# Optimization experiments

Measured on AMD Instinct MI355X. Metric: run time of the kernel, lower is better.

## Reference

```python
import jax, jax.numpy as jnp
import numpy as np

N = 50000
E = 800000
F_IN = 128
F_OUT = 128


def setup_inputs() -> dict:
    key = jax.random.key(0)
    ks = jax.random.split(key, 7)
    feature = jax.random.normal(ks[0], (N, F_IN), dtype=jnp.float32)
    self_weight = jax.random.uniform(ks[1], (N, 1), dtype=jnp.float32)
    weight = jax.random.uniform(ks[2], (E,), dtype=jnp.float32)
    src = jax.random.randint(ks[3], (E,), 0, N, dtype=jnp.int32)
    dst = jax.random.randint(ks[4], (E,), 0, N, dtype=jnp.int32)
    W = jax.random.normal(ks[5], (F_OUT, F_IN), dtype=jnp.float32) / np.sqrt(F_IN)
    b = jax.random.normal(ks[6], (F_OUT,), dtype=jnp.float32) * 0.01
    return {"feature": feature, "self_weight": self_weight, "weight": weight,
            "src": src, "dst": dst, "W": W, "b": b}


def reference(feature, self_weight, weight, src, dst, W, b):
    # messages: (w + 1) * h_src  -> [E, F_IN]
    msgs = (weight + 1.0)[:, None] * feature[src]
    # segment-sum into destination nodes -> [N, F_IN]
    agg = jax.ops.segment_sum(msgs, dst, num_segments=N)
    # self-loop affine: h * (self_weight + 1) + aggregated messages
    h = feature * (self_weight + 1.0) + agg
    # final linear: h @ W^T + b
    return h @ W.T + b
```

## Files before the change

### kernel.cpp

```cpp
#include <hip/hip_runtime.h>


#define F 128
#define NPB 32
#define CAPB 1024
#define CHUNK 4096
#define MAXNB 1600

typedef __attribute__((ext_vector_type(8))) short short8;
typedef __attribute__((ext_vector_type(4))) float f32x4;

__device__ inline unsigned short f2b(float f) {
    union { float f; unsigned u; } v; v.f = f;
    unsigned r = (v.u + 0x7fffu + ((v.u >> 16) & 1u)) >> 16;
    return (unsigned short)r;
}
__device__ inline float blo(unsigned u) { union { unsigned u; float f; } x; x.u = u << 16; return x.f; }
__device__ inline float bhi(unsigned u) { union { unsigned u; float f; } x; x.u = u & 0xffff0000u; return x.f; }

struct __align__(8) Edge { unsigned pk; float w; };

__global__ __launch_bounds__(256) void init_kernel(
    const float* __restrict__ W, unsigned short* __restrict__ wbf,
    int* __restrict__ gcur, int nb)
{
    int i = blockIdx.x * 256 + threadIdx.x;
    if (i < 4096) {
        float4 v = ((const float4*)W)[i];
        ushort4 h; h.x = f2b(v.x); h.y = f2b(v.y); h.z = f2b(v.z); h.w = f2b(v.w);
        ((ushort4*)wbf)[i] = h;
    } else if (i - 4096 < nb) {
        gcur[i - 4096] = 0;
    }
}

__global__ __launch_bounds__(256) void gemm_scatter(
    const float* __restrict__ feat, const unsigned short* __restrict__ wbf,
    const int* __restrict__ dst, const int* __restrict__ src,
    const float* __restrict__ weight,
    unsigned short* __restrict__ g, int* __restrict__ gcur,
    Edge* __restrict__ sorted, int M, int E, int SB, int NB)
{
    __shared__ __align__(16) char smem[128 * 136 * 2];
    const int tid = threadIdx.x;

    if ((int)blockIdx.x >= SB) {
        unsigned short* Wl = (unsigned short*)smem;
        const int row0 = ((int)blockIdx.x - SB) * 64;

        const int lane = tid & 63, wid = tid >> 6;
        const int m = lane & 15, quad = lane >> 4;
        const int rbase = wid * 16;
        int rr = row0 + rbase + m; if (rr >= M) rr = M - 1;
        const float* frow = feat + (size_t)rr * F;

        float4 a32[4][2];
#pragma unroll
        for (int kk = 0; kk < 4; ++kk) {
            a32[kk][0] = *(const float4*)&frow[kk * 32 + quad * 8];
            a32[kk][1] = *(const float4*)&frow[kk * 32 + quad * 8 + 4];
        }

        for (int i = tid; i < 2048; i += 256) {
            int r = i >> 4, c8 = i & 15;
            *(uint4*)&Wl[r * 136 + c8 * 8] = *(const uint4*)&wbf[r * 128 + c8 * 8];
        }

        short8 afrag[4];
#pragma unroll
        for (int kk = 0; kk < 4; ++kk) {
            afrag[kk][0] = (short)f2b(a32[kk][0].x);
            afrag[kk][1] = (short)f2b(a32[kk][0].y);
            afrag[kk][2] = (short)f2b(a32[kk][0].z);
            afrag[kk][3] = (short)f2b(a32[kk][0].w);
            afrag[kk][4] = (short)f2b(a32[kk][1].x);
            afrag[kk][5] = (short)f2b(a32[kk][1].y);
            afrag[kk][6] = (short)f2b(a32[kk][1].z);
            afrag[kk][7] = (short)f2b(a32[kk][1].w);
        }
        __syncthreads();

        f32x4 acc[8];
#pragma unroll
        for (int t = 0; t < 8; ++t) acc[t] = (f32x4){0.f, 0.f, 0.f, 0.f};

#pragma unroll
        for (int kk = 0; kk < 4; ++kk) {
            const int k0 = kk * 32 + quad * 8;
#pragma unroll
            for (int t = 0; t < 8; ++t) {
                short8 bfrag = *(const short8*)&Wl[(t * 16 + m) * 136 + k0];
                acc[t] = __builtin_amdgcn_mfma_f32_16x16x32_bf16(afrag[kk], bfrag, acc[t], 0, 0, 0);
            }
        }

#pragma unroll
        for (int reg = 0; reg < 4; ++reg) {
            int r = row0 + rbase + quad * 4 + reg;
            if (r < M) {
#pragma unroll
                for (int t = 0; t < 8; ++t)
                    g[(size_t)r * F + t * 16 + m] = f2b(acc[t][reg]);
            }
        }
    } else {
        int* hist  = (int*)smem;
        int* lbase = hist + MAXNB;
        const int e0 = (int)blockIdx.x * CHUNK;

        int dvals[CHUNK / 256];
        for (int i = tid; i < NB; i += 256) hist[i] = 0;
        __syncthreads();
#pragma unroll
        for (int j = 0; j < CHUNK / 256; ++j) {
            int e = e0 + j * 256 + tid;
            dvals[j] = (e < E) ? dst[e] : -1;
            if (dvals[j] >= 0) atomicAdd(&hist[dvals[j] >> 5], 1);
        }
        __syncthreads();
        for (int i = tid; i < NB; i += 256) {
            int c = hist[i];
            lbase[i] = c ? atomicAdd(&gcur[i], c) : 0;
            hist[i] = 0;
        }
        __syncthreads();
#pragma unroll
        for (int j = 0; j < CHUNK / 256; ++j) {
            int d = dvals[j];
            if (d >= 0) {
                int e = e0 + j * 256 + tid;
                int bkt = d >> 5;
                int pos = lbase[bkt] + atomicAdd(&hist[bkt], 1);
                if (pos < CAPB) {
                    Edge ed;
                    ed.pk = (unsigned)src[e] | ((unsigned)(d & 31) << 16);
                    ed.w = weight[e] + 1.0f;
                    sorted[(size_t)bkt * CAPB + pos] = ed;
                }
            }
        }
    }
}

__global__ __launch_bounds__(512) void bucket_gather(
    const unsigned short* __restrict__ g, const Edge* __restrict__ sorted,
    const int* __restrict__ gcur, const float* __restrict__ sw,
    const float* __restrict__ bvec, float* __restrict__ out, int M)
{
    __shared__ Edge eraw[CAPB];
    __shared__ Edge ebuf[CAPB];
    __shared__ int hcnt[NPB];
    __shared__ int off[NPB + 1];
    __shared__ int cur[NPB];

    const int b = blockIdx.x, tid = threadIdx.x;
    int cnt = gcur[b]; if (cnt > CAPB) cnt = CAPB;
    const Edge* sb = sorted + (size_t)b * CAPB;

    if (tid < NPB) hcnt[tid] = 0;
    __syncthreads();
    for (int i = tid; i < cnt; i += 512) {
        Edge e = sb[i];
        eraw[i] = e;
        atomicAdd(&hcnt[e.pk >> 16], 1);
    }
    __syncthreads();
    if (tid < NPB) {
        int v = hcnt[tid];
        int x = v;
#pragma unroll
        for (int s = 1; s < NPB; s <<= 1) {
            int t = __shfl_up(x, s, 64);
            if (tid >= s) x += t;
        }
        off[tid + 1] = x;
        if (tid == 0) off[0] = 0;
        cur[tid] = x - v;
    }
    __syncthreads();
    for (int i = tid; i < cnt; i += 512) {
        Edge e = eraw[i];
        int p = atomicAdd(&cur[e.pk >> 16], 1);
        if (p < CAPB) ebuf[p] = e;
    }
    __syncthreads();

    const int grp = tid >> 4, c = tid & 15;
    const int node = b * NPB + grp;
    if (node >= M) return;
    int p = off[grp];
    int pe = off[grp + 1]; if (pe > CAPB) pe = CAPB;

    const float4 b0 = ((const float4*)bvec)[c * 2];
    const float4 b1 = ((const float4*)bvec)[c * 2 + 1];

    float acc[8] = {0.f, 0.f, 0.f, 0.f, 0.f, 0.f, 0.f, 0.f};
    for (; p + 3 < pe; p += 4) {
        Edge e0 = ebuf[p], e1 = ebuf[p + 1], e2 = ebuf[p + 2], e3 = ebuf[p + 3];
        const uint4 r0 = *(const uint4*)(g + (size_t)(e0.pk & 0xffffu) * F + c * 8);
        const uint4 r1 = *(const uint4*)(g + (size_t)(e1.pk & 0xffffu) * F + c * 8);
        const uint4 r2 = *(const uint4*)(g + (size_t)(e2.pk & 0xffffu) * F + c * 8);
        const uint4 r3 = *(const uint4*)(g + (size_t)(e3.pk & 0xffffu) * F + c * 8);
        float w0 = e0.w, w1 = e1.w, w2 = e2.w, w3 = e3.w;
        acc[0] = fmaf(w0, blo(r0.x), acc[0]); acc[1] = fmaf(w0, bhi(r0.x), acc[1]);
        acc[2] = fmaf(w0, blo(r0.y), acc[2]); acc[3] = fmaf(w0, bhi(r0.y), acc[3]);
        acc[4] = fmaf(w0, blo(r0.z), acc[4]); acc[5] = fmaf(w0, bhi(r0.z), acc[5]);
        acc[6] = fmaf(w0, blo(r0.w), acc[6]); acc[7] = fmaf(w0, bhi(r0.w), acc[7]);
        acc[0] = fmaf(w1, blo(r1.x), acc[0]); acc[1] = fmaf(w1, bhi(r1.x), acc[1]);
        acc[2] = fmaf(w1, blo(r1.y), acc[2]); acc[3] = fmaf(w1, bhi(r1.y), acc[3]);
        acc[4] = fmaf(w1, blo(r1.z), acc[4]); acc[5] = fmaf(w1, bhi(r1.z), acc[5]);
        acc[6] = fmaf(w1, blo(r1.w), acc[6]); acc[7] = fmaf(w1, bhi(r1.w), acc[7]);
        acc[0] = fmaf(w2, blo(r2.x), acc[0]); acc[1] = fmaf(w2, bhi(r2.x), acc[1]);
        acc[2] = fmaf(w2, blo(r2.y), acc[2]); acc[3] = fmaf(w2, bhi(r2.y), acc[3]);
        acc[4] = fmaf(w2, blo(r2.z), acc[4]); acc[5] = fmaf(w2, bhi(r2.z), acc[5]);
        acc[6] = fmaf(w2, blo(r2.w), acc[6]); acc[7] = fmaf(w2, bhi(r2.w), acc[7]);
        acc[0] = fmaf(w3, blo(r3.x), acc[0]); acc[1] = fmaf(w3, bhi(r3.x), acc[1]);
        acc[2] = fmaf(w3, blo(r3.y), acc[2]); acc[3] = fmaf(w3, bhi(r3.y), acc[3]);
        acc[4] = fmaf(w3, blo(r3.z), acc[4]); acc[5] = fmaf(w3, bhi(r3.z), acc[5]);
        acc[6] = fmaf(w3, blo(r3.w), acc[6]); acc[7] = fmaf(w3, bhi(r3.w), acc[7]);
    }
    for (; p < pe; ++p) {
        Edge e0 = ebuf[p];
        const uint4 r0 = *(const uint4*)(g + (size_t)(e0.pk & 0xffffu) * F + c * 8);
        float w0 = e0.w;
        acc[0] = fmaf(w0, blo(r0.x), acc[0]); acc[1] = fmaf(w0, bhi(r0.x), acc[1]);
        acc[2] = fmaf(w0, blo(r0.y), acc[2]); acc[3] = fmaf(w0, bhi(r0.y), acc[3]);
        acc[4] = fmaf(w0, blo(r0.z), acc[4]); acc[5] = fmaf(w0, bhi(r0.z), acc[5]);
        acc[6] = fmaf(w0, blo(r0.w), acc[6]); acc[7] = fmaf(w0, bhi(r0.w), acc[7]);
    }

    const uint4 sr = *(const uint4*)(g + (size_t)node * F + c * 8);
    const float s = sw[node] + 1.0f;
    float4 o0, o1;
    o0.x = fmaf(s, blo(sr.x), b0.x) + acc[0];
    o0.y = fmaf(s, bhi(sr.x), b0.y) + acc[1];
    o0.z = fmaf(s, blo(sr.y), b0.z) + acc[2];
    o0.w = fmaf(s, bhi(sr.y), b0.w) + acc[3];
    o1.x = fmaf(s, blo(sr.z), b1.x) + acc[4];
    o1.y = fmaf(s, bhi(sr.z), b1.y) + acc[5];
    o1.z = fmaf(s, blo(sr.w), b1.z) + acc[6];
    o1.w = fmaf(s, bhi(sr.w), b1.w) + acc[7];
    float4* o = (float4*)(out + (size_t)node * F + c * 8);
    o[0] = o0; o[1] = o1;
}

extern "C" void kernel_launch(void* const* d_in, const int* in_sizes, int n_in,
                              void* d_out, int out_size, void* d_ws, size_t ws_size,
                              hipStream_t stream) {
    const float* feat   = (const float*)d_in[0];
    const float* sw     = (const float*)d_in[1];
    const float* weight = (const float*)d_in[2];
    const int*   src    = (const int*)  d_in[3];
    const int*   dst    = (const int*)  d_in[4];
    const float* W      = (const float*)d_in[5];
    const float* b      = (const float*)d_in[6];
    float* out = (float*)d_out;

    const int M = in_sizes[1];
    const int E = in_sizes[2];
    const int NB = (M + NPB - 1) / NPB;
    const int GB = (M + 63) / 64;
    const int SB = (E + CHUNK - 1) / CHUNK;

    char* ws = (char*)d_ws;
    size_t og    = 0;
    size_t owbf  = ((og   + (size_t)M * F * 2) + 255) & ~(size_t)255;
    size_t ocur  = ((owbf + (size_t)F * F * 2) + 255) & ~(size_t)255;
    size_t osort = ((ocur + (size_t)NB * 4) + 255) & ~(size_t)255;

    unsigned short* g   = (unsigned short*)(ws + og);
    unsigned short* wbf = (unsigned short*)(ws + owbf);
    int*  gcur   = (int*)(ws + ocur);
    Edge* sorted = (Edge*)(ws + osort);

    const int initN = 4096 + NB;
    init_kernel<<<(initN + 255) / 256, 256, 0, stream>>>(W, wbf, gcur, NB);
    gemm_scatter<<<SB + GB, 256, 0, stream>>>(
        feat, wbf, dst, src, weight, g, gcur, sorted, M, E, SB, NB);
    bucket_gather<<<NB, 512, 0, stream>>>(g, sorted, gcur, sw, b, out, M);
}
```

Baseline: 144.2 us.

## Replace global atomic bucket cursors with per-chunk fixed-capacity edge segments

Each scatter block now writes its edges straight into a per-chunk, per-bucket segment of fixed capacity (16) and records the counts, with no global atomics and no second pass over dst. The gather kernel prefix-sums the per-chunk counts for its bucket and assembles the edge list from up to 391 segments. This removes the global atomicAdd on bucket cursors, the two-pass scatter and the cursor zeroing in the init kernel. The cost is much sparser gather reads (one small segment per chunk per bucket) and edges dropped if any chunk-bucket pair exceeds 16 entries. It also depends on the number of chunks staying at or below 512.

```diff
diff --git a/kernel.cpp b/kernel.cpp
--- a/kernel.cpp
+++ b/kernel.cpp
@@ -4,8 +4,10 @@
 #define F 128
 #define NPB 32
 #define CAPB 1024
-#define CHUNK 4096
+#define CHUNK 2048
 #define MAXNB 1600
+#define SEGCAP 16
+#define NCHMAX 512
 
 typedef __attribute__((ext_vector_type(8))) short short8;
 typedef __attribute__((ext_vector_type(4))) float f32x4;
@@ -21,16 +23,13 @@
 struct __align__(8) Edge { unsigned pk; float w; };
 
 __global__ __launch_bounds__(256) void init_kernel(
-    const float* __restrict__ W, unsigned short* __restrict__ wbf,
-    int* __restrict__ gcur, int nb)
+    const float* __restrict__ W, unsigned short* __restrict__ wbf)
 {
     int i = blockIdx.x * 256 + threadIdx.x;
     if (i < 4096) {
         float4 v = ((const float4*)W)[i];
         ushort4 h; h.x = f2b(v.x); h.y = f2b(v.y); h.z = f2b(v.z); h.w = f2b(v.w);
         ((ushort4*)wbf)[i] = h;
-    } else if (i - 4096 < nb) {
-        gcur[i - 4096] = 0;
     }
 }
 
@@ -38,8 +37,8 @@
     const float* __restrict__ feat, const unsigned short* __restrict__ wbf,
     const int* __restrict__ dst, const int* __restrict__ src,
     const float* __restrict__ weight,
-    unsigned short* __restrict__ g, int* __restrict__ gcur,
-    Edge* __restrict__ sorted, int M, int E, int SB, int NB)
+    unsigned short* __restrict__ g, int* __restrict__ cnt,
+    Edge* __restrict__ seg, int M, int E, int SB, int NB)
 {
     __shared__ __align__(16) char smem[128 * 136 * 2];
     const int tid = threadIdx.x;
@@ -104,66 +103,87 @@
             }
         }
     } else {
-        int* hist  = (int*)smem;
-        int* lbase = hist + MAXNB;
-        const int e0 = (int)blockIdx.x * CHUNK;
-
-        int dvals[CHUNK / 256];
+        int* hist = (int*)smem;
+        const int ch = (int)blockIdx.x;
+        const int e0 = ch * CHUNK;
+
         for (int i = tid; i < NB; i += 256) hist[i] = 0;
         __syncthreads();
 #pragma unroll
         for (int j = 0; j < CHUNK / 256; ++j) {
             int e = e0 + j * 256 + tid;
-            dvals[j] = (e < E) ? dst[e] : -1;
-            if (dvals[j] >= 0) atomicAdd(&hist[dvals[j] >> 5], 1);
+            if (e < E) {
+                int d = dst[e];
+                int bkt = d >> 5;
+                Edge ed;
+                ed.pk = (unsigned)src[e] | ((unsigned)(d & 31) << 16);
+                ed.w  = weight[e] + 1.0f;
+                int pos = atomicAdd(&hist[bkt], 1);
+                if (pos < SEGCAP)
+                    seg[((size_t)ch * NB + bkt) * SEGCAP + pos] = ed;
+            }
         }
         __syncthreads();
         for (int i = tid; i < NB; i += 256) {
             int c = hist[i];
-            lbase[i] = c ? atomicAdd(&gcur[i], c) : 0;
-            hist[i] = 0;
-        }
-        __syncthreads();
-#pragma unroll
-        for (int j = 0; j < CHUNK / 256; ++j) {
-            int d = dvals[j];
-            if (d >= 0) {
-                int e = e0 + j * 256 + tid;
-                int bkt = d >> 5;
-                int pos = lbase[bkt] + atomicAdd(&hist[bkt], 1);
-                if (pos < CAPB) {
-                    Edge ed;
-                    ed.pk = (unsigned)src[e] | ((unsigned)(d & 31) << 16);
-                    ed.w = weight[e] + 1.0f;
-                    sorted[(size_t)bkt * CAPB + pos] = ed;
-                }
-            }
+            cnt[(size_t)ch * NB + i] = c > SEGCAP ? SEGCAP : c;
         }
     }
 }
 
 __global__ __launch_bounds__(512) void bucket_gather(
-    const unsigned short* __restrict__ g, const Edge* __restrict__ sorted,
-    const int* __restrict__ gcur, const float* __restrict__ sw,
-    const float* __restrict__ bvec, float* __restrict__ out, int M)
+    const unsigned short* __restrict__ g, const Edge* __restrict__ seg,
+    const int* __restrict__ cnt, const float* __restrict__ sw,
+    const float* __restrict__ bvec, float* __restrict__ out,
+    int M, int NB, int NCH)
 {
     __shared__ Edge eraw[CAPB];
     __shared__ Edge ebuf[CAPB];
+    __shared__ int ccnt[NCHMAX];
+    __shared__ int coff[NCHMAX];
+    __shared__ int wsum[8];
     __shared__ int hcnt[NPB];
     __shared__ int off[NPB + 1];
     __shared__ int cur[NPB];
+    __shared__ int tot_s;
 
     const int b = blockIdx.x, tid = threadIdx.x;
-    int cnt = gcur[b]; if (cnt > CAPB) cnt = CAPB;
-    const Edge* sb = sorted + (size_t)b * CAPB;
-
+
+    ccnt[tid] = (tid < NCH) ? cnt[(size_t)tid * NB + b] : 0;
     if (tid < NPB) hcnt[tid] = 0;
     __syncthreads();
-    for (int i = tid; i < cnt; i += 512) {
-        Edge e = sb[i];
-        eraw[i] = e;
-        atomicAdd(&hcnt[e.pk >> 16], 1);
-    }
+    {
+        int v = ccnt[tid];
+        int lane = tid & 63, wv = tid >> 6;
+        int x = v;
+#pragma unroll
+        for (int s = 1; s < 64; s <<= 1) {
+            int u = __shfl_up(x, s, 64);
+            if (lane >= s) x += u;
+        }
+        if (lane == 63) wsum[wv] = x;
+        __syncthreads();
+        int wbase = 0;
+        for (int k = 0; k < wv; ++k) wbase += wsum[k];
+        coff[tid] = x + wbase - v;
+        if (tid == 511) tot_s = x + wbase;
+    }
+    __syncthreads();
+    int cnt_total = tot_s; if (cnt_total > CAPB) cnt_total = CAPB;
+
+    {
+        int c = ccnt[tid];
+        int o = coff[tid];
+        const Edge* s0 = seg + ((size_t)tid * NB + b) * SEGCAP;
+        for (int k = 0; k < c; ++k) {
+            int p = o + k;
+            if (p < CAPB) eraw[p] = s0[k];
+        }
+    }
+    __syncthreads();
+
+    for (int i = tid; i < cnt_total; i += 512)
+        atomicAdd(&hcnt[eraw[i].pk >> 16], 1);
     __syncthreads();
     if (tid < NPB) {
         int v = hcnt[tid];
@@ -178,7 +198,7 @@
         cur[tid] = x - v;
     }
     __syncthreads();
-    for (int i = tid; i < cnt; i += 512) {
+    for (int i = tid; i < cnt_total; i += 512) {
         Edge e = eraw[i];
         int p = atomicAdd(&cur[e.pk >> 16], 1);
         if (p < CAPB) ebuf[p] = e;
@@ -265,17 +285,16 @@
     char* ws = (char*)d_ws;
     size_t og    = 0;
     size_t owbf  = ((og   + (size_t)M * F * 2) + 255) & ~(size_t)255;
-    size_t ocur  = ((owbf + (size_t)F * F * 2) + 255) & ~(size_t)255;
-    size_t osort = ((ocur + (size_t)NB * 4) + 255) & ~(size_t)255;
+    size_t ocnt  = ((owbf + (size_t)F * F * 2) + 255) & ~(size_t)255;
+    size_t oseg  = ((ocnt + (size_t)SB * NB * 4) + 255) & ~(size_t)255;
 
     unsigned short* g   = (unsigned short*)(ws + og);
     unsigned short* wbf = (unsigned short*)(ws + owbf);
-    int*  gcur   = (int*)(ws + ocur);
-    Edge* sorted = (Edge*)(ws + osort);
-
-    const int initN = 4096 + NB;
-    init_kernel<<<(initN + 255) / 256, 256, 0, stream>>>(W, wbf, gcur, NB);
+    int*  cnt = (int*)(ws + ocnt);
+    Edge* seg = (Edge*)(ws + oseg);
+
+    init_kernel<<<16, 256, 0, stream>>>(W, wbf);
     gemm_scatter<<<SB + GB, 256, 0, stream>>>(
-        feat, wbf, dst, src, weight, g, gcur, sorted, M, E, SB, NB);
-    bucket_gather<<<NB, 512, 0, stream>>>(g, sorted, gcur, sw, b, out, M);
-}
+        feat, wbf, dst, src, weight, g, cnt, seg, M, E, SB, NB);
+    bucket_gather<<<NB, 512, 0, stream>>>(g, seg, cnt, sw, b, out, M, NB, SB);
+}
```

New measurement: 158.9 us. +10.2%, slower.
